# Kernel optimization log

Measured on AMD Instinct MI355X. Metric: run time of the kernel, lower is better.

## Reference

```python
import jax, jax.numpy as jnp
import numpy as np

# Jamba mamba mixer dims
H = 4096      # hidden_size
D = 8192      # intermediate_size = mamba_expand * hidden_size
N = 16        # ssm_state_size (mamba_d_state)
K = 4         # conv_kernel_size (mamba_d_conv)
R = 256       # time_step_rank (mamba_dt_rank)
BATCH = 1
L = 2048
EPS = 1e-6


def setup_inputs() -> dict:
    key = jax.random.key(0)
    ks = jax.random.split(key, 10)
    s = 0.02
    return {
        "hidden_states": jax.random.normal(ks[0], (BATCH, L, H), jnp.float32),
        "W_in": jax.random.normal(ks[1], (2 * D, H), jnp.float32) * s,
        "conv_w": jax.random.normal(ks[2], (D, K), jnp.float32) * s,
        "conv_b": jax.random.normal(ks[3], (D,), jnp.float32) * s,
        "Wx": jax.random.normal(ks[4], (R + 2 * N, D), jnp.float32) * s,
        "dt_ln_w": jnp.ones((R,), jnp.float32),
        "b_ln_w": jnp.ones((N,), jnp.float32),
        "c_ln_w": jnp.ones((N,), jnp.float32),
        "Wdt": jax.random.normal(ks[5], (D, R), jnp.float32) * s,
        "dt_bias": jax.random.normal(ks[6], (D,), jnp.float32) * s,
        "A": -jnp.exp(jax.random.normal(ks[7], (D, N), jnp.float32) * 0.5),  # A = -exp(A_log)
        "D_param": jnp.ones((D,), jnp.float32),
        "W_out": jax.random.normal(ks[8], (H, D), jnp.float32) * s,
    }


def _rmsnorm(x, w):
    return x * jax.lax.rsqrt(jnp.mean(x * x, axis=-1, keepdims=True) + EPS) * w


def reference(hidden_states, W_in, conv_w, conv_b, Wx, dt_ln_w, b_ln_w, c_ln_w,
              Wdt, dt_bias, A, D_param, W_out):
    # in_proj -> [B, L, 2D]; split into ssm branch and gate
    proj = hidden_states @ W_in.T
    u, gate = jnp.split(proj, 2, axis=-1)

    # causal depthwise conv1d over sequence dim, then SiLU (causal_conv1d_fn)
    x = jnp.transpose(u, (0, 2, 1))  # [B, D, L]
    x = jax.lax.conv_general_dilated(
        x, conv_w[:, None, :], window_strides=(1,), padding=[(K - 1, 0)],
        dimension_numbers=("NCH", "OIH", "NCH"), feature_group_count=D)
    u = jax.nn.silu(jnp.transpose(x, (0, 2, 1)) + conv_b)  # [B, L, D]

    # x_proj -> dt / B / C with RMSNorms
    ssm_p = u @ Wx.T  # [B, L, R + 2N]
    dt, Bm, Cm = jnp.split(ssm_p, [R, R + N], axis=-1)
    dt = _rmsnorm(dt, dt_ln_w)
    Bm = _rmsnorm(Bm, b_ln_w)
    Cm = _rmsnorm(Cm, c_ln_w)

    # dt_proj (skip_bias_add: bias folded into softplus, delta_softplus=True)
    delta = jax.nn.softplus(dt @ Wdt.T + dt_bias)  # [B, L, D]

    # selective scan: state [B, D, N], recurrence over L
    def step(state, xs):
        d_t, B_t, C_t, u_t = xs  # [B,D], [B,N], [B,N], [B,D]
        dA = jnp.exp(d_t[..., None] * A)                       # [B, D, N]
        state = dA * state + (d_t * u_t)[..., None] * B_t[:, None, :]
        y_t = jnp.einsum("bdn,bn->bd", state, C_t)
        return state, y_t

    init = jnp.zeros((hidden_states.shape[0], D, N), hidden_states.dtype)
    xs = (jnp.swapaxes(delta, 0, 1), jnp.swapaxes(Bm, 0, 1),
          jnp.swapaxes(Cm, 0, 1), jnp.swapaxes(u, 0, 1))
    _, ys = jax.lax.scan(step, init, xs)  # ys: [L, B, D]

    y = jnp.swapaxes(ys, 0, 1) + u * D_param   # skip connection u * D
    y = y * jax.nn.silu(gate)                  # gated output
    return y @ W_out.T                         # out_proj -> [B, L, H]
```

## Files before the change

### kernel.cpp

```cpp
#include <hip/hip_runtime.h>
#include <stdint.h>


#define LSEQ 2048
#define HDIM 4096
#define DDIM 8192
#define NST  16
#define NPAD 384
#define NC   16
#define CLEN 128

typedef __bf16 bf16x8 __attribute__((ext_vector_type(8)));
typedef float  f32x4  __attribute__((ext_vector_type(4)));

__device__ __forceinline__ ushort f2b(float f) {
  uint32_t x = __float_as_uint(f);
  x += 0x7FFFu + ((x >> 16) & 1u);
  return (ushort)(x >> 16);
}
__device__ __forceinline__ float b2f(ushort u) {
  return __uint_as_float(((uint32_t)u) << 16);
}

__device__ __forceinline__ void gload_lds16(const ushort* g, ushort* l) {
  __builtin_amdgcn_global_load_lds(
      (const __attribute__((address_space(1))) void*)g,
      (__attribute__((address_space(3))) void*)l, 16, 0, 0);
}

__global__ __launch_bounds__(256) void cvt_kernel(const float* __restrict__ s,
                                                  ushort* __restrict__ d,
                                                  size_t n8) {
  size_t i = (size_t)blockIdx.x * 256 + threadIdx.x;
  if (i >= n8) return;
  const float4* sp = (const float4*)s;
  float4 a = sp[2 * i], b = sp[2 * i + 1];
  union { ushort us[8]; uint4 v; } u;
  u.us[0] = f2b(a.x); u.us[1] = f2b(a.y); u.us[2] = f2b(a.z); u.us[3] = f2b(a.w);
  u.us[4] = f2b(b.x); u.us[5] = f2b(b.y); u.us[6] = f2b(b.z); u.us[7] = f2b(b.w);
  ((uint4*)d)[i] = u.v;
}

template <int MODE, int OUT>
__global__ __launch_bounds__(512, 2) void gemm8p(
    const ushort* __restrict__ A, const ushort* __restrict__ Bw,
    void* __restrict__ Cv, int M, int N, int ldk, int Kc) {
  __shared__ __align__(16) ushort As[2][256 * 64];
  __shared__ __align__(16) ushort Bs[2][256 * 64];
  const int tid  = threadIdx.x;
  const int lane = tid & 63;
  const int w    = tid >> 6;
  const int wr   = w >> 2;
  const int wc   = w & 3;

  const int glob = (blockIdx.z * gridDim.y + blockIdx.y) * gridDim.x + blockIdx.x;
  const int k8 = glob & 7, j = glob >> 3;
  int mt, nt, zz;
  if (MODE == 0) {
    mt = j & 7;
    nt = k8 * (gridDim.x >> 3) + (j >> 3);
    zz = 0;
  } else {
    mt = (k8 & 1) * 4 + (j & 3);
    nt = (k8 >> 1) * 4 + ((j >> 2) & 3);
    zz = j >> 4;
  }
  const int m0 = mt * 256, n0 = nt * 256;
  const int kbeg = zz * Kc;
  float*  C  = (float*) Cv + (size_t)zz * M * N;
  ushort* Cb = (ushort*)Cv + (size_t)zz * M * N;
  const int NT = Kc >> 6;

  const int srck = (lane & 7) ^ ((lane >> 3) & 7);
  const int astripe = w >> 2, awl = w & 3;
  const int arow_st = astripe * 128 + awl * 8 + (lane >> 3);
  const ushort* Abase = A + (size_t)(m0 + arow_st) * ldk + kbeg + srck * 8;
  const int aldsb = (astripe * 128 + awl * 8) * 64;
  const int brow_st = w * 8 + (lane >> 3);
  const ushort* Bbase = Bw + (size_t)(n0 + brow_st) * ldk + kbeg + srck * 8;
  const int bldsb = (w * 8) * 64;

  const int lrow = lane & 15;
  const int kch  = lane >> 4;
  const int axor = lrow & 7;

  auto stA = [&](int buf, int kt, int q) {
    gload_lds16(Abase + (size_t)q * 32 * ldk + kt * 64,
                &As[buf][aldsb + q * 32 * 64]);
  };
  auto stB = [&](int buf, int kt, int half, int jj) {
    gload_lds16(Bbase + (size_t)(half * 128 + jj * 64) * ldk + kt * 64,
                &Bs[buf][bldsb + (half * 128 + jj * 64) * 64]);
  };
  auto rdA = [&](int buf, int mi, int sl) -> bf16x8 {
    int arow = wr * 128 + mi * 16 + lrow;
    int s4 = sl * 4 + kch;
    return *(const bf16x8*)&As[buf][arow * 64 + ((s4 ^ axor) << 3)];
  };
  auto rdB = [&](int buf, int ni, int sl) -> bf16x8 {
    int brow = wc * 64 + ni * 16 + lrow;
    int s4 = sl * 4 + kch;
    return *(const bf16x8*)&Bs[buf][brow * 64 + ((s4 ^ axor) << 3)];
  };

  f32x4 acc[8][4] = {};

  stB(0, 0, 0, 0); stB(0, 0, 0, 1); stB(0, 0, 1, 0); stB(0, 0, 1, 1);
  stA(0, 0, 0); stA(0, 0, 1); stA(0, 0, 2); stA(0, 0, 3);
  stB(1, 1, 0, 0); stB(1, 1, 0, 1); stB(1, 1, 1, 0); stB(1, 1, 1, 1);
  stA(1, 1, 0); stA(1, 1, 1);
  asm volatile("s_waitcnt vmcnt(6)" ::: "memory");
  asm volatile("s_barrier" ::: "memory");

#define PHASE(BUF, Q, STAGES)                                                 \
  {                                                                           \
    if (Q == 0) {                                                             \
      _Pragma("unroll") for (int ni = 0; ni < 4; ++ni)                        \
        _Pragma("unroll") for (int sl = 0; sl < 2; ++sl)                      \
          bfr[ni][sl] = rdB(BUF, ni, sl);                                     \
    }                                                                         \
    _Pragma("unroll") for (int m2 = 0; m2 < 2; ++m2)                          \
      _Pragma("unroll") for (int sl = 0; sl < 2; ++sl)                        \
        afr[m2][sl] = rdA(BUF, Q * 2 + m2, sl);                               \
    STAGES;                                                                   \
    asm volatile("s_barrier" ::: "memory");                                   \
    __builtin_amdgcn_s_setprio(1);                                            \
    _Pragma("unroll") for (int sl = 0; sl < 2; ++sl)                          \
      _Pragma("unroll") for (int m2 = 0; m2 < 2; ++m2)                        \
        _Pragma("unroll") for (int ni = 0; ni < 4; ++ni)                      \
          acc[Q * 2 + m2][ni] = __builtin_amdgcn_mfma_f32_16x16x32_bf16(      \
              afr[m2][sl], bfr[ni][sl], acc[Q * 2 + m2][ni], 0, 0, 0);        \
    __builtin_amdgcn_s_setprio(0);                                            \
  }

  for (int t = 0; t < NT; t += 2) {
    const int t2 = (t + 2 < NT) ? t + 2 : 0;
    const int t3 = (t + 3 < NT) ? t + 3 : 0;
    bf16x8 bfr[4][2], afr[2][2];
    PHASE(0, 0, { stA(1, t + 1, 2); stA(1, t + 1, 3); });
    asm volatile("s_barrier" ::: "memory");
    PHASE(0, 1, { stB(0, t2, 0, 0); stB(0, t2, 0, 1); });
    asm volatile("s_barrier" ::: "memory");
    PHASE(0, 2, { stB(0, t2, 1, 0); stB(0, t2, 1, 1); });
    asm volatile("s_barrier" ::: "memory");
    PHASE(0, 3, { stA(0, t2, 0); stA(0, t2, 1); });
    asm volatile("s_waitcnt vmcnt(6)" ::: "memory");
    asm volatile("s_barrier" ::: "memory");
    PHASE(1, 0, { stA(0, t2, 2); stA(0, t2, 3); });
    asm volatile("s_barrier" ::: "memory");
    PHASE(1, 1, { stB(1, t3, 0, 0); stB(1, t3, 0, 1); });
    asm volatile("s_barrier" ::: "memory");
    PHASE(1, 2, { stB(1, t3, 1, 0); stB(1, t3, 1, 1); });
    asm volatile("s_barrier" ::: "memory");
    PHASE(1, 3, { stA(1, t3, 0); stA(1, t3, 1); });
    asm volatile("s_waitcnt vmcnt(6)" ::: "memory");
    asm volatile("s_barrier" ::: "memory");
  }
#undef PHASE

  asm volatile("s_waitcnt vmcnt(0)" ::: "memory");
#pragma unroll
  for (int mi = 0; mi < 8; ++mi) {
    int row0 = m0 + wr * 128 + mi * 16 + kch * 4;
#pragma unroll
    for (int ni = 0; ni < 4; ++ni) {
      int col = n0 + wc * 64 + ni * 16 + lrow;
#pragma unroll
      for (int q_ = 0; q_ < 4; ++q_) {
        if (OUT == 0)
          C[(size_t)(row0 + q_) * N + col] = acc[mi][ni][q_];
        else
          Cb[(size_t)(row0 + q_) * N + col] = f2b(acc[mi][ni][q_]);
      }
    }
  }
}

template <int EPI>
__global__ __launch_bounds__(256) void gemm_nt(
    const ushort* __restrict__ A, const ushort* __restrict__ Bw,
    float* __restrict__ C, int M, int N, int ldk, int Kc,
    const float* __restrict__ bias) {
  __shared__ __align__(16) ushort As[128 * 64];
  __shared__ __align__(16) ushort Bs[128 * 64];
  const int tid  = threadIdx.x;
  const int lane = tid & 63;
  const int wid  = tid >> 6;
  const int wr = wid >> 1, wc = wid & 1;
  const int m0 = blockIdx.y * 128, n0 = blockIdx.x * 128;
  const int kbeg = blockIdx.z * Kc;
  C += (size_t)blockIdx.z * M * N;
  const int rr0 = tid >> 3;
  const int sl  = tid & 7;
  const int lrow = lane & 15;
  const int lks  = lane >> 4;

  f32x4 acc[4][4] = {};

  for (int k0 = kbeg; k0 < kbeg + Kc; k0 += 64) {
#pragma unroll
    for (int i = 0; i < 4; ++i) {
      int rr  = i * 32 + rr0;
      int ksl = sl ^ (rr & 7);
      const ushort* ga = A  + (size_t)(m0 + rr) * ldk + k0 + ksl * 8;
      const ushort* gb = Bw + (size_t)(n0 + rr) * ldk + k0 + ksl * 8;
      ushort* la = As + (i * 256 + (wid << 6)) * 8;
      ushort* lb = Bs + (i * 256 + (wid << 6)) * 8;
      gload_lds16(ga, la);
      gload_lds16(gb, lb);
    }
    __syncthreads();
#pragma unroll
    for (int kc = 0; kc < 2; ++kc) {
      bf16x8 av[4], bv[4];
#pragma unroll
      for (int mi = 0; mi < 4; ++mi) {
        int row = wr * 64 + mi * 16 + lrow;
        int ks  = kc * 4 + lks;
        av[mi] = *(const bf16x8*)(As + row * 64 + ((ks ^ (row & 7)) << 3));
      }
#pragma unroll
      for (int ni = 0; ni < 4; ++ni) {
        int row = wc * 64 + ni * 16 + lrow;
        int ks  = kc * 4 + lks;
        bv[ni] = *(const bf16x8*)(Bs + row * 64 + ((ks ^ (row & 7)) << 3));
      }
#pragma unroll
      for (int mi = 0; mi < 4; ++mi)
#pragma unroll
        for (int ni = 0; ni < 4; ++ni)
          acc[mi][ni] = __builtin_amdgcn_mfma_f32_16x16x32_bf16(
              av[mi], bv[ni], acc[mi][ni], 0, 0, 0);
    }
    __syncthreads();
  }

#pragma unroll
  for (int mi = 0; mi < 4; ++mi) {
    int row0 = m0 + wr * 64 + mi * 16 + (lks << 2);
#pragma unroll
    for (int ni = 0; ni < 4; ++ni) {
      int col = n0 + wc * 64 + ni * 16 + lrow;
      float bcol = 0.f;
      if (EPI == 1) bcol = bias[col];
#pragma unroll
      for (int q = 0; q < 4; ++q) {
        float v = acc[mi][ni][q];
        if (EPI == 1) {
          v += bcol;
          v = (v > 20.f) ? v : log1pf(__expf(v));
        }
        C[(size_t)(row0 + q) * N + col] = v;
      }
    }
  }
}

__global__ __launch_bounds__(256) void reduce8_kernel(
    const float* __restrict__ Cp, float* __restrict__ out) {
  size_t i = (size_t)blockIdx.x * 256 + threadIdx.x;
  const size_t MN = (size_t)LSEQ * NPAD;
  float s = 0.f;
#pragma unroll
  for (int z = 0; z < 8; ++z) s += Cp[z * MN + i];
  out[i] = s;
}

__global__ __launch_bounds__(256) void reduce2_kernel(
    const float* __restrict__ Cp, float* __restrict__ out) {
  size_t i = (size_t)blockIdx.x * 256 + threadIdx.x;
  const size_t MN4 = (size_t)LSEQ * HDIM / 4;
  float4 a = ((const float4*)Cp)[i];
  float4 b = ((const float4*)Cp)[MN4 + i];
  ((float4*)out)[i] = make_float4(a.x + b.x, a.y + b.y, a.z + b.z, a.w + b.w);
}

__global__ __launch_bounds__(256) void conv_silu_kernel(
    const float* __restrict__ ubuf, const float* __restrict__ cw,
    const float* __restrict__ cb, ushort* __restrict__ uc) {
  int d = blockIdx.x * 256 + threadIdx.x;
  int l = blockIdx.y;
  float4 w4 = ((const float4*)cw)[d];
  float wa[4] = {w4.x, w4.y, w4.z, w4.w};
  float s = cb[d];
#pragma unroll
  for (int j = 0; j < 4; ++j) {
    int li = l - 3 + j;
    if (li >= 0) s += wa[j] * ubuf[(size_t)li * DDIM + d];
  }
  float o = s / (1.f + __expf(-s));
  uc[(size_t)l * DDIM + d] = f2b(o);
}

__global__ __launch_bounds__(64) void norms_kernel(
    const float* __restrict__ ssmp, const float* __restrict__ dtw,
    const float* __restrict__ bw, const float* __restrict__ cwn,
    ushort* __restrict__ dtn, float* __restrict__ Bn, float* __restrict__ Cn) {
  int l = blockIdx.x, lane = threadIdx.x;
  const float* row = ssmp + (size_t)l * NPAD;
  float4 v = ((const float4*)row)[lane];
  float va[4] = {v.x, v.y, v.z, v.w};
  float ss = va[0]*va[0] + va[1]*va[1] + va[2]*va[2] + va[3]*va[3];
#pragma unroll
  for (int m = 32; m >= 1; m >>= 1) ss += __shfl_xor(ss, m);
  float rs = rsqrtf(ss * (1.f / 256.f) + 1e-6f);
  float4 w = ((const float4*)dtw)[lane];
  float wa[4] = {w.x, w.y, w.z, w.w};
  union { ushort us[4]; uint2 v2; } o;
#pragma unroll
  for (int j = 0; j < 4; ++j) o.us[j] = f2b(va[j] * rs * wa[j]);
  ((uint2*)(dtn + (size_t)l * 256))[lane] = o.v2;

  int g = lane & 15;
  float bv = row[256 + g], cv = row[272 + g];
  float bs = bv * bv, cs = cv * cv;
#pragma unroll
  for (int m = 8; m >= 1; m >>= 1) {
    bs += __shfl_xor(bs, m);
    cs += __shfl_xor(cs, m);
  }
  if (lane < 16) {
    Bn[(size_t)l * NST + lane] = bv * rsqrtf(bs * (1.f / 16.f) + 1e-6f) * bw[lane];
    Cn[(size_t)l * NST + lane] = cv * rsqrtf(cs * (1.f / 16.f) + 1e-6f) * cwn[lane];
  }
}

__global__ __launch_bounds__(256) void scan_phase1(
    const float* __restrict__ delta, const ushort* __restrict__ uc,
    const float* __restrict__ Bn, const float* __restrict__ Am,
    float* __restrict__ Sbuf, float* __restrict__ Pbuf) {
  __shared__ float sB[CLEN * NST];
  const int tid = threadIdx.x;
  const int d = blockIdx.x * 256 + tid;
  const int c = blockIdx.y, l0 = c * CLEN;
  {
    const float4* bsrc = (const float4*)(Bn + (size_t)l0 * NST);
    float4* bdst = (float4*)sB;
    for (int i = tid; i < CLEN * NST / 4; i += 256) bdst[i] = bsrc[i];
  }
  __syncthreads();
  float A[16];
#pragma unroll
  for (int j = 0; j < 4; ++j) {
    float4 a4 = ((const float4*)(Am + (size_t)d * NST))[j];
    A[4*j] = a4.x; A[4*j+1] = a4.y; A[4*j+2] = a4.z; A[4*j+3] = a4.w;
  }
  float st[16] = {};
  float sd = 0.f;
  const size_t base = (size_t)l0 * DDIM + d;
  float dx0 = delta[base],            dx1 = delta[base + DDIM];
  float ux0 = b2f(uc[base]),          ux1 = b2f(uc[base + DDIM]);
  for (int l = 0; l < CLEN; l += 2) {
    int lp = (l + 2 < CLEN) ? l + 2 : CLEN - 2;
    float dxn0 = delta[base + (size_t)lp * DDIM];
    float dxn1 = delta[base + (size_t)(lp + 1) * DDIM];
    float uxn0 = b2f(uc[base + (size_t)lp * DDIM]);
    float uxn1 = b2f(uc[base + (size_t)(lp + 1) * DDIM]);
    sd += dx0;
    float dxu = dx0 * ux0;
#pragma unroll
    for (int n = 0; n < 16; ++n)
      st[n] = fmaf(__expf(dx0 * A[n]), st[n], dxu * sB[l * NST + n]);
    sd += dx1;
    dxu = dx1 * ux1;
#pragma unroll
    for (int n = 0; n < 16; ++n)
      st[n] = fmaf(__expf(dx1 * A[n]), st[n], dxu * sB[(l + 1) * NST + n]);
    dx0 = dxn0; dx1 = dxn1; ux0 = uxn0; ux1 = uxn1;
  }
  float4* Sd = (float4*)(Sbuf + ((size_t)c * DDIM + d) * NST);
  float4* Pd = (float4*)(Pbuf + ((size_t)c * DDIM + d) * NST);
#pragma unroll
  for (int j = 0; j < 4; ++j) {
    Sd[j] = make_float4(st[4*j], st[4*j+1], st[4*j+2], st[4*j+3]);
    Pd[j] = make_float4(__expf(A[4*j] * sd),   __expf(A[4*j+1] * sd),
                        __expf(A[4*j+2] * sd), __expf(A[4*j+3] * sd));
  }
}

__global__ __launch_bounds__(256) void scan_phase2(
    const float* __restrict__ Sbuf, float* __restrict__ Pbuf) {
  size_t t = (size_t)blockIdx.x * 256 + threadIdx.x;
  const size_t stride = (size_t)DDIM * NST;
  float s = 0.f;
  for (int c = 0; c < NC; ++c) {
    float P = Pbuf[c * stride + t];
    float S = Sbuf[c * stride + t];
    Pbuf[c * stride + t] = s;
    s = fmaf(P, s, S);
  }
}

__global__ __launch_bounds__(256) void scan_phase3(
    const float* __restrict__ delta, const ushort* __restrict__ uc,
    const float* __restrict__ Bn, const float* __restrict__ Cn,
    const float* __restrict__ Am, const float* __restrict__ Ibuf,
    const ushort* __restrict__ gbuf, const float* __restrict__ Dp,
    ushort* __restrict__ yg) {
  __shared__ float sB[CLEN * NST];
  __shared__ float sC[CLEN * NST];
  const int tid = threadIdx.x;
  const int d = blockIdx.x * 256 + tid;
  const int c = blockIdx.y, l0 = c * CLEN;
  {
    const float4* bsrc = (const float4*)(Bn + (size_t)l0 * NST);
    const float4* csrc = (const float4*)(Cn + (size_t)l0 * NST);
    float4* bdst = (float4*)sB;
    float4* cdst = (float4*)sC;
    for (int i = tid; i < CLEN * NST / 4; i += 256) {
      bdst[i] = bsrc[i];
      cdst[i] = csrc[i];
    }
  }
  __syncthreads();
  float A[16], st[16];
#pragma unroll
  for (int j = 0; j < 4; ++j) {
    float4 a4 = ((const float4*)(Am + (size_t)d * NST))[j];
    A[4*j] = a4.x; A[4*j+1] = a4.y; A[4*j+2] = a4.z; A[4*j+3] = a4.w;
    float4 s4 = ((const float4*)(Ibuf + ((size_t)c * DDIM + d) * NST))[j];
    st[4*j] = s4.x; st[4*j+1] = s4.y; st[4*j+2] = s4.z; st[4*j+3] = s4.w;
  }
  const float Dpd = Dp[d];
  const size_t base = (size_t)l0 * DDIM + d;
  float dx0 = delta[base],   dx1 = delta[base + DDIM];
  float ux0 = b2f(uc[base]), ux1 = b2f(uc[base + DDIM]);
  float g0  = b2f(gbuf[base]), g1 = b2f(gbuf[base + DDIM]);
  for (int l = 0; l < CLEN; l += 2) {
    int lp = (l + 2 < CLEN) ? l + 2 : CLEN - 2;
    float dxn0 = delta[base + (size_t)lp * DDIM];
    float dxn1 = delta[base + (size_t)(lp + 1) * DDIM];
    float uxn0 = b2f(uc[base + (size_t)lp * DDIM]);
    float uxn1 = b2f(uc[base + (size_t)(lp + 1) * DDIM]);
    float gn0  = b2f(gbuf[base + (size_t)lp * DDIM]);
    float gn1  = b2f(gbuf[base + (size_t)(lp + 1) * DDIM]);
    {
      float dxu = dx0 * ux0, y0 = 0.f, y1 = 0.f;
#pragma unroll
      for (int n = 0; n < 16; n += 2) {
        st[n]   = fmaf(__expf(dx0 * A[n]),   st[n],   dxu * sB[l * NST + n]);
        st[n+1] = fmaf(__expf(dx0 * A[n+1]), st[n+1], dxu * sB[l * NST + n+1]);
        y0 = fmaf(st[n],   sC[l * NST + n],   y0);
        y1 = fmaf(st[n+1], sC[l * NST + n+1], y1);
      }
      float o = (y0 + y1 + ux0 * Dpd) * (g0 / (1.f + __expf(-g0)));
      yg[base + (size_t)l * DDIM] = f2b(o);
    }
    {
      float dxu = dx1 * ux1, y0 = 0.f, y1 = 0.f;
#pragma unroll
      for (int n = 0; n < 16; n += 2) {
        st[n]   = fmaf(__expf(dx1 * A[n]),   st[n],   dxu * sB[(l+1) * NST + n]);
        st[n+1] = fmaf(__expf(dx1 * A[n+1]), st[n+1], dxu * sB[(l+1) * NST + n+1]);
        y0 = fmaf(st[n],   sC[(l+1) * NST + n],   y0);
        y1 = fmaf(st[n+1], sC[(l+1) * NST + n+1], y1);
      }
      float o = (y0 + y1 + ux1 * Dpd) * (g1 / (1.f + __expf(-g1)));
      yg[base + (size_t)(l + 1) * DDIM] = f2b(o);
    }
    dx0 = dxn0; dx1 = dxn1; ux0 = uxn0; ux1 = uxn1; g0 = gn0; g1 = gn1;
  }
}

extern "C" void kernel_launch(void* const* d_in, const int* in_sizes, int n_in,
                              void* d_out, int out_size, void* d_ws, size_t ws_size,
                              hipStream_t stream) {
  (void)in_sizes; (void)n_in; (void)out_size; (void)ws_size;
  const float* hs   = (const float*)d_in[0];
  const float* W_in = (const float*)d_in[1];
  const float* cw   = (const float*)d_in[2];
  const float* cb   = (const float*)d_in[3];
  const float* Wx   = (const float*)d_in[4];
  const float* dtw  = (const float*)d_in[5];
  const float* bw   = (const float*)d_in[6];
  const float* cwn  = (const float*)d_in[7];
  const float* Wdt  = (const float*)d_in[8];
  const float* dtb  = (const float*)d_in[9];
  const float* Am   = (const float*)d_in[10];
  const float* Dp   = (const float*)d_in[11];
  const float* Wout = (const float*)d_in[12];
  float* out = (float*)d_out;

  char* ws = (char*)d_ws;
  const size_t MB = 1ull << 20;
  ushort* win_b  = (ushort*)(ws);
  float*  delta  = (float*) (ws);
  ushort* wout_b = (ushort*)(ws + 64 * MB);
  float*  ubuf   = (float*) (ws + 128 * MB);
  float*  Cp     = (float*) (ws + 128 * MB);
  float*  Cp2    = (float*) (ws + 128 * MB);
  float*  Sbuf   = (float*) (ws + 152 * MB);
  float*  Pbuf   = (float*) (ws + 160 * MB);
  ushort* gbuf   = (ushort*)(ws + 192 * MB);
  ushort* hs_b   = (ushort*)(ws + 256 * MB);
  ushort* wxp_b  = (ushort*)(ws + 272 * MB);
  ushort* wdt_b  = (ushort*)(ws + 278 * MB);
  ushort* ucv    = (ushort*)(ws + 282 * MB);
  float*  ssmp   = (float*) (ws + 314 * MB);
  ushort* dtn    = (ushort*)(ws + 317 * MB);
  float*  Bn     = (float*) (ws + 318 * MB);
  float*  Cn     = (float*) (ws + 318 * MB + 131072);
  ushort* yg     = (ushort*)(ws + 319 * MB);

  cvt_kernel<<<67108864 / 2048, 256, 0, stream>>>(W_in, win_b, 67108864 / 8);
  cvt_kernel<<<8388608 / 2048, 256, 0, stream>>>(hs, hs_b, 8388608 / 8);
  cvt_kernel<<<2359296 / 2048, 256, 0, stream>>>(Wx, wxp_b, 2359296 / 8);
  hipMemsetAsync((char*)wxp_b + 4718592, 0, 1572864, stream);
  cvt_kernel<<<2097152 / 2048, 256, 0, stream>>>(Wdt, wdt_b, 2097152 / 8);

  gemm8p<0, 0><<<dim3(32, 8), 512, 0, stream>>>(hs_b, win_b, ubuf,
                                                2048, DDIM, 4096, 4096);
  gemm8p<0, 1><<<dim3(32, 8), 512, 0, stream>>>(hs_b, win_b + (size_t)DDIM * 4096,
                                                gbuf, 2048, DDIM, 4096, 4096);
  cvt_kernel<<<33554432 / 2048, 256, 0, stream>>>(Wout, wout_b, 33554432 / 8);

  conv_silu_kernel<<<dim3(32, 2048), 256, 0, stream>>>(ubuf, cw, cb, ucv);

  gemm_nt<0><<<dim3(3, 16, 8), 256, 0, stream>>>(ucv, wxp_b, Cp,
                                                 2048, NPAD, 8192, 1024, nullptr);
  reduce8_kernel<<<3072, 256, 0, stream>>>(Cp, ssmp);

  norms_kernel<<<2048, 64, 0, stream>>>(ssmp, dtw, bw, cwn, dtn, Bn, Cn);

  gemm_nt<1><<<dim3(64, 16), 256, 0, stream>>>(dtn, wdt_b, delta,
                                               2048, DDIM, 256, 256, dtb);

  scan_phase1<<<dim3(32, NC), 256, 0, stream>>>(delta, ucv, Bn, Am, Sbuf, Pbuf);
  scan_phase2<<<512, 256, 0, stream>>>(Sbuf, Pbuf);
  scan_phase3<<<dim3(32, NC), 256, 0, stream>>>(delta, ucv, Bn, Cn, Am, Pbuf,
                                                gbuf, Dp, yg);

  gemm8p<1, 0><<<dim3(16, 8, 2), 512, 0, stream>>>(yg, wout_b, Cp2,
                                                   2048, HDIM, 8192, 4096);
  reduce2_kernel<<<(LSEQ * HDIM / 4) / 256, 256, 0, stream>>>(Cp2, out);
}
```

Measured before the change: 882.0 us.

## Software-pipeline LDS reads in gemm8p, store intermediates in bf16, fuse reduce into norms

Restructures the 8-wave GEMM main loop so LDS fragment reads for the next quarter are double-buffered in registers and overlap the current MFMA block, dropping several barriers per K-step. The u projection output and delta are now stored as bf16 instead of fp32, halving traffic for the conv and scan kernels. The split-K reduction for x_proj is folded into the norms kernel, removing a launch and an intermediate buffer. The conv kernel now processes 16 timesteps per thread with a sliding window. These changes add register pressure and more bf16 rounding of u and delta.

New measurement: 813.3 us. -7.8%, faster.

```diff
diff --git a/kernel.cpp b/kernel.cpp
--- a/kernel.cpp
+++ b/kernel.cpp
@@ -67,8 +67,6 @@
   }
   const int m0 = mt * 256, n0 = nt * 256;
   const int kbeg = zz * Kc;
-  float*  C  = (float*) Cv + (size_t)zz * M * N;
-  ushort* Cb = (ushort*)Cv + (size_t)zz * M * N;
   const int NT = Kc >> 6;
 
   const int srck = (lane & 7) ^ ((lane >> 3) & 7);
@@ -104,61 +102,76 @@
   };
 
   f32x4 acc[8][4] = {};
-
-  stB(0, 0, 0, 0); stB(0, 0, 0, 1); stB(0, 0, 1, 0); stB(0, 0, 1, 1);
-  stA(0, 0, 0); stA(0, 0, 1); stA(0, 0, 2); stA(0, 0, 3);
-  stB(1, 1, 0, 0); stB(1, 1, 0, 1); stB(1, 1, 1, 0); stB(1, 1, 1, 1);
-  stA(1, 1, 0); stA(1, 1, 1);
-  asm volatile("s_waitcnt vmcnt(6)" ::: "memory");
-  asm volatile("s_barrier" ::: "memory");
-
-#define PHASE(BUF, Q, STAGES)                                                 \
-  {                                                                           \
-    if (Q == 0) {                                                             \
-      _Pragma("unroll") for (int ni = 0; ni < 4; ++ni)                        \
-        _Pragma("unroll") for (int sl = 0; sl < 2; ++sl)                      \
-          bfr[ni][sl] = rdB(BUF, ni, sl);                                     \
-    }                                                                         \
-    _Pragma("unroll") for (int m2 = 0; m2 < 2; ++m2)                          \
+  bf16x8 afr[2][2][2];
+  bf16x8 bfr[2][4][2];
+
+#define RDAQ(BUF, Q, AP)                                                      \
+  { _Pragma("unroll") for (int m2 = 0; m2 < 2; ++m2)                          \
       _Pragma("unroll") for (int sl = 0; sl < 2; ++sl)                        \
-        afr[m2][sl] = rdA(BUF, Q * 2 + m2, sl);                               \
-    STAGES;                                                                   \
-    asm volatile("s_barrier" ::: "memory");                                   \
+        afr[AP][m2][sl] = rdA(BUF, (Q) * 2 + m2, sl); }
+#define RDBALL(BUF, BP)                                                       \
+  { _Pragma("unroll") for (int ni = 0; ni < 4; ++ni)                          \
+      _Pragma("unroll") for (int sl = 0; sl < 2; ++sl)                        \
+        bfr[BP][ni][sl] = rdB(BUF, ni, sl); }
+#define MFMA16(MQ, AP, BP)                                                    \
+  { asm volatile("s_barrier" ::: "memory");                                   \
     __builtin_amdgcn_s_setprio(1);                                            \
     _Pragma("unroll") for (int sl = 0; sl < 2; ++sl)                          \
       _Pragma("unroll") for (int m2 = 0; m2 < 2; ++m2)                        \
         _Pragma("unroll") for (int ni = 0; ni < 4; ++ni)                      \
-          acc[Q * 2 + m2][ni] = __builtin_amdgcn_mfma_f32_16x16x32_bf16(      \
-              afr[m2][sl], bfr[ni][sl], acc[Q * 2 + m2][ni], 0, 0, 0);        \
-    __builtin_amdgcn_s_setprio(0);                                            \
-  }
+          acc[(MQ) * 2 + m2][ni] = __builtin_amdgcn_mfma_f32_16x16x32_bf16(   \
+              afr[AP][m2][sl], bfr[BP][ni][sl], acc[(MQ) * 2 + m2][ni],       \
+              0, 0, 0);                                                       \
+    __builtin_amdgcn_s_setprio(0); }
+
+  stB(0, 0, 0, 0); stB(0, 0, 0, 1); stB(0, 0, 1, 0); stB(0, 0, 1, 1);
+  stA(0, 0, 0); stA(0, 0, 1); stA(0, 0, 2); stA(0, 0, 3);
+  stB(1, 1, 0, 0); stB(1, 1, 0, 1); stB(1, 1, 1, 0); stB(1, 1, 1, 1);
+  stA(1, 1, 0); stA(1, 1, 1); stA(1, 1, 2); stA(1, 1, 3);
+  asm volatile("s_waitcnt vmcnt(8)" ::: "memory");
+  asm volatile("s_barrier" ::: "memory");
+  RDBALL(0, 0);
+  RDAQ(0, 0, 1);
 
   for (int t = 0; t < NT; t += 2) {
     const int t2 = (t + 2 < NT) ? t + 2 : 0;
     const int t3 = (t + 3 < NT) ? t + 3 : 0;
-    bf16x8 bfr[4][2], afr[2][2];
-    PHASE(0, 0, { stA(1, t + 1, 2); stA(1, t + 1, 3); });
-    asm volatile("s_barrier" ::: "memory");
-    PHASE(0, 1, { stB(0, t2, 0, 0); stB(0, t2, 0, 1); });
-    asm volatile("s_barrier" ::: "memory");
-    PHASE(0, 2, { stB(0, t2, 1, 0); stB(0, t2, 1, 1); });
-    asm volatile("s_barrier" ::: "memory");
-    PHASE(0, 3, { stA(0, t2, 0); stA(0, t2, 1); });
+    RDAQ(0, 1, 0);
+    stB(0, t2, 0, 0); stB(0, t2, 0, 1);
+    MFMA16(0, 1, 0);
+    RDAQ(0, 2, 1);
+    stB(0, t2, 1, 0); stB(0, t2, 1, 1);
+    MFMA16(1, 0, 0);
+    RDAQ(0, 3, 0);
+    stA(0, t2, 0); stA(0, t2, 1);
+    MFMA16(2, 1, 0);
     asm volatile("s_waitcnt vmcnt(6)" ::: "memory");
-    asm volatile("s_barrier" ::: "memory");
-    PHASE(1, 0, { stA(0, t2, 2); stA(0, t2, 3); });
-    asm volatile("s_barrier" ::: "memory");
-    PHASE(1, 1, { stB(1, t3, 0, 0); stB(1, t3, 0, 1); });
-    asm volatile("s_barrier" ::: "memory");
-    PHASE(1, 2, { stB(1, t3, 1, 0); stB(1, t3, 1, 1); });
-    asm volatile("s_barrier" ::: "memory");
-    PHASE(1, 3, { stA(1, t3, 0); stA(1, t3, 1); });
+    RDBALL(1, 1);
+    RDAQ(1, 0, 1);
+    stA(0, t2, 2); stA(0, t2, 3);
+    MFMA16(3, 0, 0);
+    RDAQ(1, 1, 0);
+    stB(1, t3, 0, 0); stB(1, t3, 0, 1);
+    MFMA16(0, 1, 1);
+    RDAQ(1, 2, 1);
+    stB(1, t3, 1, 0); stB(1, t3, 1, 1);
+    MFMA16(1, 0, 1);
+    RDAQ(1, 3, 0);
+    stA(1, t3, 0); stA(1, t3, 1);
+    MFMA16(2, 1, 1);
     asm volatile("s_waitcnt vmcnt(6)" ::: "memory");
-    asm volatile("s_barrier" ::: "memory");
-  }
-#undef PHASE
+    RDBALL(0, 0);
+    RDAQ(0, 0, 1);
+    stA(1, t3, 2); stA(1, t3, 3);
+    MFMA16(3, 0, 1);
+  }
+#undef RDAQ
+#undef RDBALL
+#undef MFMA16
 
   asm volatile("s_waitcnt vmcnt(0)" ::: "memory");
+  float*  C  = (float*) Cv + (size_t)zz * M * N;
+  ushort* Cb = (ushort*)Cv + (size_t)zz * M * N;
 #pragma unroll
   for (int mi = 0; mi < 8; ++mi) {
     int row0 = m0 + wr * 128 + mi * 16 + kch * 4;
@@ -176,10 +189,10 @@
   }
 }
 
-template <int EPI>
+template <int EPI, int OBF>
 __global__ __launch_bounds__(256) void gemm_nt(
     const ushort* __restrict__ A, const ushort* __restrict__ Bw,
-    float* __restrict__ C, int M, int N, int ldk, int Kc,
+    void* __restrict__ Cv, int M, int N, int ldk, int Kc,
     const float* __restrict__ bias) {
   __shared__ __align__(16) ushort As[128 * 64];
   __shared__ __align__(16) ushort Bs[128 * 64];
@@ -189,7 +202,8 @@
   const int wr = wid >> 1, wc = wid & 1;
   const int m0 = blockIdx.y * 128, n0 = blockIdx.x * 128;
   const int kbeg = blockIdx.z * Kc;
-  C += (size_t)blockIdx.z * M * N;
+  float*  C  = (float*) Cv + (size_t)blockIdx.z * M * N;
+  ushort* Cb = (ushort*)Cv + (size_t)blockIdx.z * M * N;
   const int rr0 = tid >> 3;
   const int sl  = tid & 7;
   const int lrow = lane & 15;
@@ -250,20 +264,11 @@
           v += bcol;
           v = (v > 20.f) ? v : log1pf(__expf(v));
         }
-        C[(size_t)(row0 + q) * N + col] = v;
+        if (OBF == 0) C [(size_t)(row0 + q) * N + col] = v;
+        else          Cb[(size_t)(row0 + q) * N + col] = f2b(v);
       }
     }
   }
-}
-
-__global__ __launch_bounds__(256) void reduce8_kernel(
-    const float* __restrict__ Cp, float* __restrict__ out) {
-  size_t i = (size_t)blockIdx.x * 256 + threadIdx.x;
-  const size_t MN = (size_t)LSEQ * NPAD;
-  float s = 0.f;
-#pragma unroll
-  for (int z = 0; z < 8; ++z) s += Cp[z * MN + i];
-  out[i] = s;
 }
 
 __global__ __launch_bounds__(256) void reduce2_kernel(
@@ -276,43 +281,57 @@
 }
 
 __global__ __launch_bounds__(256) void conv_silu_kernel(
-    const float* __restrict__ ubuf, const float* __restrict__ cw,
+    const ushort* __restrict__ ub, const float* __restrict__ cw,
     const float* __restrict__ cb, ushort* __restrict__ uc) {
   int d = blockIdx.x * 256 + threadIdx.x;
-  int l = blockIdx.y;
+  int l0 = blockIdx.y * 16;
   float4 w4 = ((const float4*)cw)[d];
-  float wa[4] = {w4.x, w4.y, w4.z, w4.w};
-  float s = cb[d];
-#pragma unroll
-  for (int j = 0; j < 4; ++j) {
-    int li = l - 3 + j;
-    if (li >= 0) s += wa[j] * ubuf[(size_t)li * DDIM + d];
-  }
-  float o = s / (1.f + __expf(-s));
-  uc[(size_t)l * DDIM + d] = f2b(o);
+  float bsum = cb[d];
+  float xm3 = (l0 >= 3) ? b2f(ub[(size_t)(l0 - 3) * DDIM + d]) : 0.f;
+  float xm2 = (l0 >= 2) ? b2f(ub[(size_t)(l0 - 2) * DDIM + d]) : 0.f;
+  float xm1 = (l0 >= 1) ? b2f(ub[(size_t)(l0 - 1) * DDIM + d]) : 0.f;
+#pragma unroll
+  for (int i = 0; i < 16; ++i) {
+    int l = l0 + i;
+    float xc = b2f(ub[(size_t)l * DDIM + d]);
+    float s = bsum + w4.x * xm3 + w4.y * xm2 + w4.z * xm1 + w4.w * xc;
+    float o = s / (1.f + __expf(-s));
+    uc[(size_t)l * DDIM + d] = f2b(o);
+    xm3 = xm2; xm2 = xm1; xm1 = xc;
+  }
 }
 
 __global__ __launch_bounds__(64) void norms_kernel(
-    const float* __restrict__ ssmp, const float* __restrict__ dtw,
+    const float* __restrict__ Cp, const float* __restrict__ dtw,
     const float* __restrict__ bw, const float* __restrict__ cwn,
     ushort* __restrict__ dtn, float* __restrict__ Bn, float* __restrict__ Cn) {
   int l = blockIdx.x, lane = threadIdx.x;
-  const float* row = ssmp + (size_t)l * NPAD;
-  float4 v = ((const float4*)row)[lane];
-  float va[4] = {v.x, v.y, v.z, v.w};
+  const size_t MN = (size_t)LSEQ * NPAD;
+  const float* row = Cp + (size_t)l * NPAD;
+  float va[4] = {0.f, 0.f, 0.f, 0.f};
+#pragma unroll
+  for (int z = 0; z < 8; ++z) {
+    float4 v = ((const float4*)(row + z * MN))[lane];
+    va[0] += v.x; va[1] += v.y; va[2] += v.z; va[3] += v.w;
+  }
   float ss = va[0]*va[0] + va[1]*va[1] + va[2]*va[2] + va[3]*va[3];
 #pragma unroll
   for (int m = 32; m >= 1; m >>= 1) ss += __shfl_xor(ss, m);
   float rs = rsqrtf(ss * (1.f / 256.f) + 1e-6f);
-  float4 w = ((const float4*)dtw)[lane];
-  float wa[4] = {w.x, w.y, w.z, w.w};
+  float4 wv = ((const float4*)dtw)[lane];
+  float wa[4] = {wv.x, wv.y, wv.z, wv.w};
   union { ushort us[4]; uint2 v2; } o;
 #pragma unroll
-  for (int j = 0; j < 4; ++j) o.us[j] = f2b(va[j] * rs * wa[j]);
+  for (int jj = 0; jj < 4; ++jj) o.us[jj] = f2b(va[jj] * rs * wa[jj]);
   ((uint2*)(dtn + (size_t)l * 256))[lane] = o.v2;
 
   int g = lane & 15;
-  float bv = row[256 + g], cv = row[272 + g];
+  float bv = 0.f, cv = 0.f;
+#pragma unroll
+  for (int z = 0; z < 8; ++z) {
+    bv += row[z * MN + 256 + g];
+    cv += row[z * MN + 272 + g];
+  }
   float bs = bv * bv, cs = cv * cv;
 #pragma unroll
   for (int m = 8; m >= 1; m >>= 1) {
@@ -326,7 +345,7 @@
 }
 
 __global__ __launch_bounds__(256) void scan_phase1(
-    const float* __restrict__ delta, const ushort* __restrict__ uc,
+    const ushort* __restrict__ delta, const ushort* __restrict__ uc,
     const float* __restrict__ Bn, const float* __restrict__ Am,
     float* __restrict__ Sbuf, float* __restrict__ Pbuf) {
   __shared__ float sB[CLEN * NST];
@@ -341,19 +360,19 @@
   __syncthreads();
   float A[16];
 #pragma unroll
-  for (int j = 0; j < 4; ++j) {
-    float4 a4 = ((const float4*)(Am + (size_t)d * NST))[j];
-    A[4*j] = a4.x; A[4*j+1] = a4.y; A[4*j+2] = a4.z; A[4*j+3] = a4.w;
+  for (int jj = 0; jj < 4; ++jj) {
+    float4 a4 = ((const float4*)(Am + (size_t)d * NST))[jj];
+    A[4*jj] = a4.x; A[4*jj+1] = a4.y; A[4*jj+2] = a4.z; A[4*jj+3] = a4.w;
   }
   float st[16] = {};
   float sd = 0.f;
   const size_t base = (size_t)l0 * DDIM + d;
-  float dx0 = delta[base],            dx1 = delta[base + DDIM];
-  float ux0 = b2f(uc[base]),          ux1 = b2f(uc[base + DDIM]);
+  float dx0 = b2f(delta[base]),  dx1 = b2f(delta[base + DDIM]);
+  float ux0 = b2f(uc[base]),     ux1 = b2f(uc[base + DDIM]);
   for (int l = 0; l < CLEN; l += 2) {
     int lp = (l + 2 < CLEN) ? l + 2 : CLEN - 2;
-    float dxn0 = delta[base + (size_t)lp * DDIM];
-    float dxn1 = delta[base + (size_t)(lp + 1) * DDIM];
+    float dxn0 = b2f(delta[base + (size_t)lp * DDIM]);
+    float dxn1 = b2f(delta[base + (size_t)(lp + 1) * DDIM]);
     float uxn0 = b2f(uc[base + (size_t)lp * DDIM]);
     float uxn1 = b2f(uc[base + (size_t)(lp + 1) * DDIM]);
     sd += dx0;
@@ -371,10 +390,10 @@
   float4* Sd = (float4*)(Sbuf + ((size_t)c * DDIM + d) * NST);
   float4* Pd = (float4*)(Pbuf + ((size_t)c * DDIM + d) * NST);
 #pragma unroll
-  for (int j = 0; j < 4; ++j) {
-    Sd[j] = make_float4(st[4*j], st[4*j+1], st[4*j+2], st[4*j+3]);
-    Pd[j] = make_float4(__expf(A[4*j] * sd),   __expf(A[4*j+1] * sd),
-                        __expf(A[4*j+2] * sd), __expf(A[4*j+3] * sd));
+  for (int jj = 0; jj < 4; ++jj) {
+    Sd[jj] = make_float4(st[4*jj], st[4*jj+1], st[4*jj+2], st[4*jj+3]);
+    Pd[jj] = make_float4(__expf(A[4*jj] * sd),   __expf(A[4*jj+1] * sd),
+                         __expf(A[4*jj+2] * sd), __expf(A[4*jj+3] * sd));
   }
 }
 
@@ -392,7 +411,7 @@
 }
 
 __global__ __launch_bounds__(256) void scan_phase3(
-    const float* __restrict__ delta, const ushort* __restrict__ uc,
+    const ushort* __restrict__ delta, const ushort* __restrict__ uc,
     const float* __restrict__ Bn, const float* __restrict__ Cn,
     const float* __restrict__ Am, const float* __restrict__ Ibuf,
     const ushort* __restrict__ gbuf, const float* __restrict__ Dp,
@@ -415,21 +434,21 @@
   __syncthreads();
   float A[16], st[16];
 #pragma unroll
-  for (int j = 0; j < 4; ++j) {
-    float4 a4 = ((const float4*)(Am + (size_t)d * NST))[j];
-    A[4*j] = a4.x; A[4*j+1] = a4.y; A[4*j+2] = a4.z; A[4*j+3] = a4.w;
-    float4 s4 = ((const float4*)(Ibuf + ((size_t)c * DDIM + d) * NST))[j];
-    st[4*j] = s4.x; st[4*j+1] = s4.y; st[4*j+2] = s4.z; st[4*j+3] = s4.w;
+  for (int jj = 0; jj < 4; ++jj) {
+    float4 a4 = ((const float4*)(Am + (size_t)d * NST))[jj];
+    A[4*jj] = a4.x; A[4*jj+1] = a4.y; A[4*jj+2] = a4.z; A[4*jj+3] = a4.w;
+    float4 s4 = ((const float4*)(Ibuf + ((size_t)c * DDIM + d) * NST))[jj];
+    st[4*jj] = s4.x; st[4*jj+1] = s4.y; st[4*jj+2] = s4.z; st[4*jj+3] = s4.w;
   }
   const float Dpd = Dp[d];
   const size_t base = (size_t)l0 * DDIM + d;
-  float dx0 = delta[base],   dx1 = delta[base + DDIM];
-  float ux0 = b2f(uc[base]), ux1 = b2f(uc[base + DDIM]);
-  float g0  = b2f(gbuf[base]), g1 = b2f(gbuf[base + DDIM]);
+  float dx0 = b2f(delta[base]),   dx1 = b2f(delta[base + DDIM]);
+  float ux0 = b2f(uc[base]),      ux1 = b2f(uc[base + DDIM]);
+  float g0  = b2f(gbuf[base]),    g1  = b2f(gbuf[base + DDIM]);
   for (int l = 0; l < CLEN; l += 2) {
     int lp = (l + 2 < CLEN) ? l + 2 : CLEN - 2;
-    float dxn0 = delta[base + (size_t)lp * DDIM];
-    float dxn1 = delta[base + (size_t)(lp + 1) * DDIM];
+    float dxn0 = b2f(delta[base + (size_t)lp * DDIM]);
+    float dxn1 = b2f(delta[base + (size_t)(lp + 1) * DDIM]);
     float uxn0 = b2f(uc[base + (size_t)lp * DDIM]);
     float uxn1 = b2f(uc[base + (size_t)(lp + 1) * DDIM]);
     float gn0  = b2f(gbuf[base + (size_t)lp * DDIM]);
@@ -483,10 +502,10 @@
 
   char* ws = (char*)d_ws;
   const size_t MB = 1ull << 20;
-  ushort* win_b  = (ushort*)(ws);
-  float*  delta  = (float*) (ws);
-  ushort* wout_b = (ushort*)(ws + 64 * MB);
-  float*  ubuf   = (float*) (ws + 128 * MB);
+  ushort* win_b   = (ushort*)(ws);
+  ushort* delta_b = (ushort*)(ws);
+  ushort* wout_b  = (ushort*)(ws + 64 * MB);
+  ushort* ubuf   = (ushort*)(ws + 128 * MB);
   float*  Cp     = (float*) (ws + 128 * MB);
   float*  Cp2    = (float*) (ws + 128 * MB);
   float*  Sbuf   = (float*) (ws + 152 * MB);
@@ -496,7 +515,6 @@
   ushort* wxp_b  = (ushort*)(ws + 272 * MB);
   ushort* wdt_b  = (ushort*)(ws + 278 * MB);
   ushort* ucv    = (ushort*)(ws + 282 * MB);
-  float*  ssmp   = (float*) (ws + 314 * MB);
   ushort* dtn    = (ushort*)(ws + 317 * MB);
   float*  Bn     = (float*) (ws + 318 * MB);
   float*  Cn     = (float*) (ws + 318 * MB + 131072);
@@ -508,26 +526,25 @@
   hipMemsetAsync((char*)wxp_b + 4718592, 0, 1572864, stream);
   cvt_kernel<<<2097152 / 2048, 256, 0, stream>>>(Wdt, wdt_b, 2097152 / 8);
 
-  gemm8p<0, 0><<<dim3(32, 8), 512, 0, stream>>>(hs_b, win_b, ubuf,
+  gemm8p<0, 1><<<dim3(32, 8), 512, 0, stream>>>(hs_b, win_b, ubuf,
                                                 2048, DDIM, 4096, 4096);
   gemm8p<0, 1><<<dim3(32, 8), 512, 0, stream>>>(hs_b, win_b + (size_t)DDIM * 4096,
                                                 gbuf, 2048, DDIM, 4096, 4096);
   cvt_kernel<<<33554432 / 2048, 256, 0, stream>>>(Wout, wout_b, 33554432 / 8);
 
-  conv_silu_kernel<<<dim3(32, 2048), 256, 0, stream>>>(ubuf, cw, cb, ucv);
-
-  gemm_nt<0><<<dim3(3, 16, 8), 256, 0, stream>>>(ucv, wxp_b, Cp,
-                                                 2048, NPAD, 8192, 1024, nullptr);
-  reduce8_kernel<<<3072, 256, 0, stream>>>(Cp, ssmp);
-
-  norms_kernel<<<2048, 64, 0, stream>>>(ssmp, dtw, bw, cwn, dtn, Bn, Cn);
-
-  gemm_nt<1><<<dim3(64, 16), 256, 0, stream>>>(dtn, wdt_b, delta,
-                                               2048, DDIM, 256, 256, dtb);
-
-  scan_phase1<<<dim3(32, NC), 256, 0, stream>>>(delta, ucv, Bn, Am, Sbuf, Pbuf);
+  conv_silu_kernel<<<dim3(32, 128), 256, 0, stream>>>(ubuf, cw, cb, ucv);
+
+  gemm_nt<0, 0><<<dim3(3, 16, 8), 256, 0, stream>>>(ucv, wxp_b, Cp,
+                                                    2048, NPAD, 8192, 1024,
+                                                    nullptr);
+  norms_kernel<<<2048, 64, 0, stream>>>(Cp, dtw, bw, cwn, dtn, Bn, Cn);
+
+  gemm_nt<1, 1><<<dim3(64, 16), 256, 0, stream>>>(dtn, wdt_b, delta_b,
+                                                  2048, DDIM, 256, 256, dtb);
+
+  scan_phase1<<<dim3(32, NC), 256, 0, stream>>>(delta_b, ucv, Bn, Am, Sbuf, Pbuf);
   scan_phase2<<<512, 256, 0, stream>>>(Sbuf, Pbuf);
-  scan_phase3<<<dim3(32, NC), 256, 0, stream>>>(delta, ucv, Bn, Cn, Am, Pbuf,
+  scan_phase3<<<dim3(32, NC), 256, 0, stream>>>(delta_b, ucv, Bn, Cn, Am, Pbuf,
                                                 gbuf, Dp, yg);
 
   gemm8p<1, 0><<<dim3(16, 8, 2), 512, 0, stream>>>(yg, wout_b, Cp2,
```
